# Optimization experiments

Measured on AMD Instinct MI355X. Metric: run time of the kernel, lower is better.

Reference implementation:

```python
import jax, jax.numpy as jnp
import numpy as np

N_NODES = 50000
N_EDGES = 800000
IN_FEATS, N_HIDDEN, N_CLASSES = 128, 128, 64
N_LAYERS = 3  # total GraphConv layers = N_LAYERS + 1


def setup_inputs() -> dict:
    key = jax.random.key(0)
    ks = jax.random.split(key, 16)
    features = jax.random.normal(ks[0], (N_NODES, IN_FEATS), dtype=jnp.float32)
    src = jax.random.randint(ks[1], (N_EDGES,), 0, N_NODES, dtype=jnp.int32)
    dst = jax.random.randint(ks[2], (N_EDGES,), 0, N_NODES, dtype=jnp.int32)
    def lin(k, fan_in, fan_out):
        s = 1.0 / np.sqrt(fan_in)
        return jax.random.uniform(k, (fan_in, fan_out), jnp.float32, -s, s)
    dims = [IN_FEATS] + [N_HIDDEN] * N_LAYERS + [N_CLASSES]
    inp = {"features": features, "src": src, "dst": dst}
    for i in range(len(dims) - 1):
        inp[f"W{i}"] = lin(ks[3 + i], dims[i], dims[i + 1])
        inp[f"b{i}"] = jnp.zeros((dims[i + 1],), jnp.float32)
    inp["Wp"] = lin(ks[10], N_CLASSES, 1)
    inp["bp"] = jnp.zeros((1,), jnp.float32)
    inp["Wv"] = lin(ks[11], N_CLASSES, 1)
    inp["bv"] = jnp.zeros((1,), jnp.float32)
    return inp


def _graph_conv(h, src, dst, norm_src, norm_dst, W, b, activate):
    # DGL GraphConv, norm='both': D_out^{-1/2} A D_in^{-1/2} X W + b
    h = h * norm_src  # [N, d]
    msg = h[src]      # [E, d] gather
    agg = jax.ops.segment_sum(msg, dst, num_segments=N_NODES)  # [N, d] scatter-add
    out = agg * norm_dst @ W + b
    return jax.nn.relu(out) if activate else out


def reference(features, src, dst, W0, b0, W1, b1, W2, b2, W3, b3, Wp, bp, Wv, bv):
    ones = jnp.ones((N_EDGES,), jnp.float32)
    out_deg = jax.ops.segment_sum(ones, src, num_segments=N_NODES)
    in_deg = jax.ops.segment_sum(ones, dst, num_segments=N_NODES)
    norm_src = jnp.clip(out_deg, 1.0) ** -0.5  # [N]
    norm_dst = jnp.clip(in_deg, 1.0) ** -0.5
    norm_src = norm_src[:, None]
    norm_dst = norm_dst[:, None]
    Ws = [W0, W1, W2, W3]
    bs = [b0, b1, b2, b3]
    h = features
    for i in range(4):
        h = _graph_conv(h, src, dst, norm_src, norm_dst, Ws[i], bs[i], activate=(i < 3))
    mN = jnp.sum(h, axis=0, keepdims=True)  # readout_nodes sum -> [1, n_classes]
    PI = h @ Wp + bp   # [N, 1]
    V = mN @ Wv + bv   # [1, 1]
    return (PI, V)
```

## Files before the change

### kernel.cpp

```cpp
#include <hip/hip_runtime.h>
#include <cstddef>

#define N_NODES 50000
#define N_EDGES 800000
#define NBUK    196
#define NBLK    256
#define EPB     3125
#define HEAD_BLOCKS 3136

typedef unsigned u32;
typedef unsigned short u16;
typedef __attribute__((ext_vector_type(8))) short bf16x8;
typedef __attribute__((ext_vector_type(4))) float f32x4;

__device__ __forceinline__ float bflo(u32 u) { return __uint_as_float(u << 16); }
__device__ __forceinline__ float bfhi(u32 u) { return __uint_as_float(u & 0xFFFF0000u); }
__device__ __forceinline__ u32 f2bf(float f) {
    u32 u = __float_as_uint(f);
    return (u + 0x7FFFu + ((u >> 16) & 1u)) >> 16;
}
__device__ __forceinline__ u32 packbf2(float a, float b) { return f2bf(a) | (f2bf(b) << 16); }

#define OFF_NS    0u
#define OFF_ND    200000u
#define OFF_RS    400000u
#define OFF_ES    600016u
#define OFF_CNTD  3800016u
#define OFF_CNTS  4000720u
#define OFF_TOTD  4201424u
#define OFF_TOTS  4202208u
#define OFF_BASED 4202992u
#define OFF_BASES 4203776u
#define OFF_VP    4204560u
#define OFF_DB    4217104u
#define OFF_SB    10617104u
#define OFF_T0    13817104u
#define OFF_T1    26617104u
#define OFF_TA    39417104u
#define OFF_TT    52217104u

__global__ __launch_bounds__(256)
void p1_kernel(const int* __restrict__ src, const int* __restrict__ dst,
               u32* __restrict__ cntD, u32* __restrict__ cntS) {
    __shared__ u32 dc[NBUK], sc[NBUK];
    int b = blockIdx.x, tid = threadIdx.x;
    if (tid < NBUK) { dc[tid] = 0; sc[tid] = 0; }
    __syncthreads();
    int lo = b * EPB, hi = lo + EPB;
    for (int e = lo + tid; e < hi; e += 256) {
        atomicAdd(&dc[dst[e] >> 8], 1u);
        atomicAdd(&sc[src[e] >> 8], 1u);
    }
    __syncthreads();
    if (tid < NBUK) {
        cntD[b * NBUK + tid] = dc[tid];
        cntS[b * NBUK + tid] = sc[tid];
    }
}

__global__ __launch_bounds__(256)
void p2a_kernel(u32* __restrict__ cntD, u32* __restrict__ cntS,
                u32* __restrict__ totD, u32* __restrict__ totS) {
    __shared__ u32 sc[256];
    int k = blockIdx.x, tid = threadIdx.x;
    u32 v = cntD[tid * NBUK + k];
    sc[tid] = v;
    __syncthreads();
    for (int o = 1; o < 256; o <<= 1) {
        u32 t = (tid >= o) ? sc[tid - o] : 0u;
        __syncthreads(); sc[tid] += t; __syncthreads();
    }
    cntD[tid * NBUK + k] = sc[tid] - v;
    if (tid == 255) totD[k] = sc[255];
    __syncthreads();
    v = cntS[tid * NBUK + k];
    sc[tid] = v;
    __syncthreads();
    for (int o = 1; o < 256; o <<= 1) {
        u32 t = (tid >= o) ? sc[tid - o] : 0u;
        __syncthreads(); sc[tid] += t; __syncthreads();
    }
    cntS[tid * NBUK + k] = sc[tid] - v;
    if (tid == 255) totS[k] = sc[255];
}

__global__ __launch_bounds__(256)
void p2b_kernel(const u32* __restrict__ totD, const u32* __restrict__ totS,
                u32* __restrict__ baseD, u32* __restrict__ baseS, u32* __restrict__ rs) {
    __shared__ u32 sc[256];
    int tid = threadIdx.x;
    u32 v = (tid < NBUK) ? totD[tid] : 0u;
    sc[tid] = v;
    __syncthreads();
    for (int o = 1; o < 256; o <<= 1) {
        u32 t = (tid >= o) ? sc[tid - o] : 0u;
        __syncthreads(); sc[tid] += t; __syncthreads();
    }
    if (tid < NBUK) baseD[tid] = sc[tid] - v;
    __syncthreads();
    v = (tid < NBUK) ? totS[tid] : 0u;
    sc[tid] = v;
    __syncthreads();
    for (int o = 1; o < 256; o <<= 1) {
        u32 t = (tid >= o) ? sc[tid - o] : 0u;
        __syncthreads(); sc[tid] += t; __syncthreads();
    }
    if (tid < NBUK) baseS[tid] = sc[tid] - v;
    if (tid == 0) rs[N_NODES] = N_EDGES;
}

__global__ __launch_bounds__(256)
void p3_kernel(const int* __restrict__ src, const int* __restrict__ dst,
               const u32* __restrict__ cntD, const u32* __restrict__ cntS,
               const u32* __restrict__ baseD, const u32* __restrict__ baseS,
               int2* __restrict__ db, int* __restrict__ sb) {
    __shared__ u32 od[NBUK], os[NBUK];
    int b = blockIdx.x, tid = threadIdx.x;
    if (tid < NBUK) {
        od[tid] = baseD[tid] + cntD[b * NBUK + tid];
        os[tid] = baseS[tid] + cntS[b * NBUK + tid];
    }
    __syncthreads();
    int lo = b * EPB, hi = lo + EPB;
    for (int e = lo + tid; e < hi; e += 256) {
        int s = src[e], d = dst[e];
        u32 p = atomicAdd(&od[d >> 8], 1u);
        db[p] = make_int2(s, d);
        u32 q = atomicAdd(&os[s >> 8], 1u);
        sb[q] = s;
    }
}

__global__ __launch_bounds__(256)
void p4d_kernel(const int2* __restrict__ db, const u32* __restrict__ totD,
                const u32* __restrict__ baseD, float* __restrict__ nd,
                u32* __restrict__ rs, int* __restrict__ es) {
    __shared__ u32 hist[256], sc[256], off[256];
    int k = blockIdx.x, tid = threadIdx.x;
    hist[tid] = 0;
    __syncthreads();
    u32 nEd = totD[k], base = baseD[k];
    for (u32 i = tid; i < nEd; i += 256)
        atomicAdd(&hist[db[base + i].y & 255], 1u);
    __syncthreads();
    u32 v = hist[tid];
    sc[tid] = v;
    __syncthreads();
    for (int o = 1; o < 256; o <<= 1) {
        u32 t = (tid >= o) ? sc[tid - o] : 0u;
        __syncthreads(); sc[tid] += t; __syncthreads();
    }
    u32 pf = sc[tid] - v;
    int node = k * 256 + tid;
    if (node < N_NODES) {
        rs[node] = base + pf;
        u32 c = v < 1u ? 1u : v;
        nd[node] = rsqrtf((float)c);
    }
    off[tid] = base + pf;
    __syncthreads();
    for (u32 i = tid; i < nEd; i += 256) {
        int2 p = db[base + i];
        u32 pos = atomicAdd(&off[p.y & 255], 1u);
        es[pos] = p.x;
    }
}

__global__ __launch_bounds__(256)
void p4sp_kernel(const int* __restrict__ sb, const u32* __restrict__ totS,
                 const u32* __restrict__ baseS, float* __restrict__ ns,
                 const float* __restrict__ feat, u16* __restrict__ hS) {
    __shared__ u32 hist[256];
    __shared__ float sns[256];
    int k = blockIdx.x, tid = threadIdx.x;
    hist[tid] = 0;
    __syncthreads();
    u32 n = totS[k], base = baseS[k];
    for (u32 i = tid; i < n; i += 256)
        atomicAdd(&hist[sb[base + i] & 255], 1u);
    __syncthreads();
    int node = k * 256 + tid;
    {
        u32 c = hist[tid]; if (c < 1u) c = 1u;
        float s = rsqrtf((float)c);
        sns[tid] = s;
        if (node < N_NODES) ns[node] = s;
    }
    __syncthreads();
    for (int i = tid; i < 256 * 32; i += 256) {
        int r = i >> 5, c4 = i & 31;
        int g = k * 256 + r;
        if (g >= N_NODES) break;
        float s = sns[r];
        float4 v = *(const float4*)&feat[(size_t)g * 128 + c4 * 4];
        uint2 o;
        o.x = packbf2(s * v.x, s * v.y);
        o.y = packbf2(s * v.z, s * v.w);
        *(uint2*)&hS[(size_t)g * 128 + c4 * 4] = o;
    }
}

__global__ __launch_bounds__(256)
void agg128_kernel(const u16* __restrict__ h, const u32* __restrict__ rs,
                   const int* __restrict__ es, u16* __restrict__ agg) {
    int node = blockIdx.x * 4 + (threadIdx.x >> 6);
    int lane = threadIdx.x & 63;
    int grp = lane >> 4;
    int q = lane & 15;
    const uint4* hp = (const uint4*)h;
    u32 s0 = rs[node], s1 = rs[node + 1];
    u32 deg = s1 - s0;
    u32 last = deg ? deg - 1u : 0u;
    float acc[8] = {0.f, 0.f, 0.f, 0.f, 0.f, 0.f, 0.f, 0.f};
    for (u32 b = 0; b < deg; b += 16) {
        u32 p0 = b + grp, p1 = b + 4 + grp, p2 = b + 8 + grp, p3 = b + 12 + grp;
        float m0 = p0 < deg ? 1.f : 0.f;  u32 x0 = p0 < deg ? p0 : last;
        float m1 = p1 < deg ? 1.f : 0.f;  u32 x1 = p1 < deg ? p1 : last;
        float m2 = p2 < deg ? 1.f : 0.f;  u32 x2 = p2 < deg ? p2 : last;
        float m3 = p3 < deg ? 1.f : 0.f;  u32 x3 = p3 < deg ? p3 : last;
        int e0 = es[s0 + x0], e1 = es[s0 + x1];
        int e2 = es[s0 + x2], e3 = es[s0 + x3];
        uint4 a = hp[(size_t)e0 * 16 + q];
        uint4 bb = hp[(size_t)e1 * 16 + q];
        uint4 c = hp[(size_t)e2 * 16 + q];
        uint4 d = hp[(size_t)e3 * 16 + q];
        acc[0] += m0 * bflo(a.x) + m1 * bflo(bb.x) + m2 * bflo(c.x) + m3 * bflo(d.x);
        acc[1] += m0 * bfhi(a.x) + m1 * bfhi(bb.x) + m2 * bfhi(c.x) + m3 * bfhi(d.x);
        acc[2] += m0 * bflo(a.y) + m1 * bflo(bb.y) + m2 * bflo(c.y) + m3 * bflo(d.y);
        acc[3] += m0 * bfhi(a.y) + m1 * bfhi(bb.y) + m2 * bfhi(c.y) + m3 * bfhi(d.y);
        acc[4] += m0 * bflo(a.z) + m1 * bflo(bb.z) + m2 * bflo(c.z) + m3 * bflo(d.z);
        acc[5] += m0 * bfhi(a.z) + m1 * bfhi(bb.z) + m2 * bfhi(c.z) + m3 * bfhi(d.z);
        acc[6] += m0 * bflo(a.w) + m1 * bflo(bb.w) + m2 * bflo(c.w) + m3 * bflo(d.w);
        acc[7] += m0 * bfhi(a.w) + m1 * bfhi(bb.w) + m2 * bfhi(c.w) + m3 * bfhi(d.w);
    }
    #pragma unroll
    for (int j = 0; j < 8; ++j) {
        acc[j] += __shfl_xor(acc[j], 16, 64);
        acc[j] += __shfl_xor(acc[j], 32, 64);
    }
    if (lane < 16) {
        uint4 pk;
        pk.x = packbf2(acc[0], acc[1]);
        pk.y = packbf2(acc[2], acc[3]);
        pk.z = packbf2(acc[4], acc[5]);
        pk.w = packbf2(acc[6], acc[7]);
        *(uint4*)&agg[(size_t)node * 128 + q * 8] = pk;
    }
}

template <int NCOL, int MODE>
__global__ __launch_bounds__(256)
void mfma_gemm_kernel(const u16* __restrict__ Ab, const float* __restrict__ W,
                      const float* __restrict__ bias, const float* __restrict__ ns,
                      const float* __restrict__ nd, u16* __restrict__ C) {
    constexpr int NT = NCOL / 16;
    constexpr int WROW = 136;
    constexpr int CROW = NCOL + 4;
    __shared__ u16 Wt[NCOL * WROW];
    __shared__ float Cl[4][16 * CROW];
    int tid = threadIdx.x;
    int w = tid >> 6, lane = tid & 63;
    int rowbase = blockIdx.x * 64 + w * 16;

    for (int i = tid; i < 64 * NCOL; i += 256) {
        int k2 = i / NCOL, c = i % NCOL;
        float w0 = W[(size_t)(2 * k2) * NCOL + c];
        float w1 = W[(size_t)(2 * k2 + 1) * NCOL + c];
        *(u32*)&Wt[c * WROW + 2 * k2] = packbf2(w0, w1);
    }
    __syncthreads();

    int m = lane & 15, kb = lane >> 4;
    int arow = rowbase + m;
    if (arow > N_NODES - 1) arow = N_NODES - 1;
    f32x4 acc[NT];
    #pragma unroll
    for (int nt = 0; nt < NT; ++nt) acc[nt] = (f32x4){0.f, 0.f, 0.f, 0.f};

    #pragma unroll
    for (int ks = 0; ks < 4; ++ks) {
        int k0 = ks * 32 + kb * 8;
        bf16x8 a = *(const bf16x8*)&Ab[(size_t)arow * 128 + k0];
        #pragma unroll
        for (int nt = 0; nt < NT; ++nt) {
            bf16x8 b = *(const bf16x8*)&Wt[(nt * 16 + m) * WROW + k0];
            acc[nt] = __builtin_amdgcn_mfma_f32_16x16x32_bf16(a, b, acc[nt], 0, 0, 0);
        }
    }

    #pragma unroll
    for (int nt = 0; nt < NT; ++nt)
        #pragma unroll
        for (int reg = 0; reg < 4; ++reg)
            Cl[w][(kb * 4 + reg) * CROW + nt * 16 + m] = acc[nt][reg];
    __syncthreads();

    constexpr int CQ = NCOL / 4;
    for (int i = lane; i < 16 * CQ; i += 64) {
        int r = i / CQ, c4 = (i % CQ) * 4;
        int row = rowbase + r;
        if (row < N_NODES) {
            float4 o = *(float4*)&Cl[w][r * CROW + c4];
            if (MODE == 0) {
                float sd = nd[row], ss = ns[row];
                o.x = ss * fmaxf(sd * o.x + bias[c4 + 0], 0.f);
                o.y = ss * fmaxf(sd * o.y + bias[c4 + 1], 0.f);
                o.z = ss * fmaxf(sd * o.z + bias[c4 + 2], 0.f);
                o.w = ss * fmaxf(sd * o.w + bias[c4 + 3], 0.f);
            }
            uint2 pk = {packbf2(o.x, o.y), packbf2(o.z, o.w)};
            *(uint2*)&C[(size_t)row * NCOL + c4] = pk;
        }
    }
}

__global__ __launch_bounds__(256)
void l3head_kernel(const u16* __restrict__ t, const u32* __restrict__ rs,
                   const int* __restrict__ es, const float* __restrict__ nd,
                   const float* __restrict__ b3, const float* __restrict__ Wp,
                   const float* __restrict__ Wv, const float* __restrict__ bp,
                   float* __restrict__ out, float* __restrict__ vpart) {
    __shared__ float sv;
    if (threadIdx.x == 0) sv = 0.f;
    __syncthreads();
    int lane = threadIdx.x & 63;
    int wvid = threadIdx.x >> 6;
    int oct = lane >> 3;
    int q = lane & 7;
    const uint4* hp = (const uint4*)t;
    float4 b3a = ((const float4*)b3)[q * 2];
    float4 b3b = ((const float4*)b3)[q * 2 + 1];
    float4 wpa = ((const float4*)Wp)[q * 2];
    float4 wpb = ((const float4*)Wp)[q * 2 + 1];
    float4 wva = ((const float4*)Wv)[q * 2];
    float4 wvb = ((const float4*)Wv)[q * 2 + 1];
    float bpv = bp[0];
    float vacc = 0.f;
    for (int n = blockIdx.x * 4 + wvid; n < N_NODES; n += HEAD_BLOCKS * 4) {
        u32 s0 = rs[n], s1 = rs[n + 1];
        u32 deg = s1 - s0;
        u32 last = deg ? deg - 1u : 0u;
        float acc[8] = {0.f, 0.f, 0.f, 0.f, 0.f, 0.f, 0.f, 0.f};
        for (u32 b = 0; b < deg; b += 32) {
            u32 p0 = b + oct, p1 = b + 8 + oct, p2 = b + 16 + oct, p3 = b + 24 + oct;
            float m0 = p0 < deg ? 1.f : 0.f;  u32 x0 = p0 < deg ? p0 : last;
            float m1 = p1 < deg ? 1.f : 0.f;  u32 x1 = p1 < deg ? p1 : last;
            float m2 = p2 < deg ? 1.f : 0.f;  u32 x2 = p2 < deg ? p2 : last;
            float m3 = p3 < deg ? 1.f : 0.f;  u32 x3 = p3 < deg ? p3 : last;
            int e0 = es[s0 + x0], e1 = es[s0 + x1];
            int e2 = es[s0 + x2], e3 = es[s0 + x3];
            uint4 a = hp[(size_t)e0 * 8 + q];
            uint4 bb = hp[(size_t)e1 * 8 + q];
            uint4 c = hp[(size_t)e2 * 8 + q];
            uint4 d = hp[(size_t)e3 * 8 + q];
            acc[0] += m0 * bflo(a.x) + m1 * bflo(bb.x) + m2 * bflo(c.x) + m3 * bflo(d.x);
            acc[1] += m0 * bfhi(a.x) + m1 * bfhi(bb.x) + m2 * bfhi(c.x) + m3 * bfhi(d.x);
            acc[2] += m0 * bflo(a.y) + m1 * bflo(bb.y) + m2 * bflo(c.y) + m3 * bflo(d.y);
            acc[3] += m0 * bfhi(a.y) + m1 * bfhi(bb.y) + m2 * bfhi(c.y) + m3 * bfhi(d.y);
            acc[4] += m0 * bflo(a.z) + m1 * bflo(bb.z) + m2 * bflo(c.z) + m3 * bflo(d.z);
            acc[5] += m0 * bfhi(a.z) + m1 * bfhi(bb.z) + m2 * bfhi(c.z) + m3 * bfhi(d.z);
            acc[6] += m0 * bflo(a.w) + m1 * bflo(bb.w) + m2 * bflo(c.w) + m3 * bflo(d.w);
            acc[7] += m0 * bfhi(a.w) + m1 * bfhi(bb.w) + m2 * bfhi(c.w) + m3 * bfhi(d.w);
        }
        #pragma unroll
        for (int j = 0; j < 8; ++j) {
            acc[j] += __shfl_xor(acc[j], 8, 64);
            acc[j] += __shfl_xor(acc[j], 16, 64);
            acc[j] += __shfl_xor(acc[j], 32, 64);
        }
        float ndv = nd[n];
        float h0 = ndv * acc[0] + b3a.x, h1 = ndv * acc[1] + b3a.y;
        float h2 = ndv * acc[2] + b3a.z, h3 = ndv * acc[3] + b3a.w;
        float h4 = ndv * acc[4] + b3b.x, h5 = ndv * acc[5] + b3b.y;
        float h6 = ndv * acc[6] + b3b.z, h7 = ndv * acc[7] + b3b.w;
        float p  = h0 * wpa.x + h1 * wpa.y + h2 * wpa.z + h3 * wpa.w
                 + h4 * wpb.x + h5 * wpb.y + h6 * wpb.z + h7 * wpb.w;
        float vv = h0 * wva.x + h1 * wva.y + h2 * wva.z + h3 * wva.w
                 + h4 * wvb.x + h5 * wvb.y + h6 * wvb.z + h7 * wvb.w;
        p  += __shfl_xor(p, 1, 64);  p  += __shfl_xor(p, 2, 64);  p  += __shfl_xor(p, 4, 64);
        vv += __shfl_xor(vv, 1, 64); vv += __shfl_xor(vv, 2, 64); vv += __shfl_xor(vv, 4, 64);
        if (lane == 0) { out[n] = p + bpv; vacc += vv; }
    }
    if (lane == 0) atomicAdd(&sv, vacc);
    __syncthreads();
    if (threadIdx.x == 0) vpart[blockIdx.x] = sv;
}

__global__ __launch_bounds__(256)
void vred_kernel(const float* __restrict__ vpart, const float* __restrict__ bv,
                 float* __restrict__ out) {
    float v = 0.f;
    for (int i = threadIdx.x; i < HEAD_BLOCKS; i += 256) v += vpart[i];
    #pragma unroll
    for (int off = 32; off; off >>= 1) v += __shfl_down(v, off, 64);
    __shared__ float s[4];
    if ((threadIdx.x & 63) == 0) s[threadIdx.x >> 6] = v;
    __syncthreads();
    if (threadIdx.x == 0) out[N_NODES] = s[0] + s[1] + s[2] + s[3] + bv[0];
}

extern "C" void kernel_launch(void* const* d_in, const int* in_sizes, int n_in,
                              void* d_out, int out_size, void* d_ws, size_t ws_size,
                              hipStream_t stream) {
    const float* feat = (const float*)d_in[0];
    const int*   src  = (const int*)d_in[1];
    const int*   dst  = (const int*)d_in[2];
    const float* W0 = (const float*)d_in[3];  const float* b0 = (const float*)d_in[4];
    const float* W1 = (const float*)d_in[5];  const float* b1 = (const float*)d_in[6];
    const float* W2 = (const float*)d_in[7];  const float* b2 = (const float*)d_in[8];
    const float* W3 = (const float*)d_in[9];  const float* b3 = (const float*)d_in[10];
    const float* Wp = (const float*)d_in[11]; const float* bp = (const float*)d_in[12];
    const float* Wv = (const float*)d_in[13]; const float* bv = (const float*)d_in[14];
    float* out = (float*)d_out;
    char*  wsb = (char*)d_ws;

    float* ns    = (float*)(wsb + OFF_NS);
    float* nd    = (float*)(wsb + OFF_ND);
    u32*   rs    = (u32*)(wsb + OFF_RS);
    int*   es    = (int*)(wsb + OFF_ES);
    u32*   cntD  = (u32*)(wsb + OFF_CNTD);
    u32*   cntS  = (u32*)(wsb + OFF_CNTS);
    u32*   totD  = (u32*)(wsb + OFF_TOTD);
    u32*   totS  = (u32*)(wsb + OFF_TOTS);
    u32*   baseD = (u32*)(wsb + OFF_BASED);
    u32*   baseS = (u32*)(wsb + OFF_BASES);
    float* vpart = (float*)(wsb + OFF_VP);
    int2*  db    = (int2*)(wsb + OFF_DB);
    int*   sb    = (int*)(wsb + OFF_SB);
    u16*   T0    = (u16*)(wsb + OFF_T0);
    u16*   T1    = (u16*)(wsb + OFF_T1);
    u16*   TA    = (u16*)(wsb + OFF_TA);
    u16*   Tt    = (u16*)(wsb + OFF_TT);

    p1_kernel<<<NBLK, 256, 0, stream>>>(src, dst, cntD, cntS);
    p2a_kernel<<<NBUK, 256, 0, stream>>>(cntD, cntS, totD, totS);
    p2b_kernel<<<1, 256, 0, stream>>>(totD, totS, baseD, baseS, rs);
    p3_kernel<<<NBLK, 256, 0, stream>>>(src, dst, cntD, cntS, baseD, baseS, db, sb);
    p4d_kernel<<<NBUK, 256, 0, stream>>>(db, totD, baseD, nd, rs, es);
    p4sp_kernel<<<NBUK, 256, 0, stream>>>(sb, totS, baseS, ns, feat, T0);

    agg128_kernel<<<12500, 256, 0, stream>>>(T0, rs, es, TA);
    mfma_gemm_kernel<128, 0><<<782, 256, 0, stream>>>(TA, W0, b0, ns, nd, T1);
    agg128_kernel<<<12500, 256, 0, stream>>>(T1, rs, es, TA);
    mfma_gemm_kernel<128, 0><<<782, 256, 0, stream>>>(TA, W1, b1, ns, nd, T0);
    agg128_kernel<<<12500, 256, 0, stream>>>(T0, rs, es, TA);
    mfma_gemm_kernel<128, 0><<<782, 256, 0, stream>>>(TA, W2, b2, ns, nd, T1);
    mfma_gemm_kernel<64, 1><<<782, 256, 0, stream>>>(T1, W3, b3, ns, nd, Tt);
    l3head_kernel<<<HEAD_BLOCKS, 256, 0, stream>>>(Tt, rs, es, nd, b3, Wp, Wv, bp, out, vpart);
    vred_kernel<<<1, 256, 0, stream>>>(vpart, bv, out);
}
```

Before: 350.6 us.

## Compress edge index buffers to narrow types and drop masked aggregation tails

Source indices in the CSR edge list are now stored as u16, since node ids fit in 16 bits. The bucketing intermediates are packed too: src<<8 | dst-low-byte goes into one u32, and the src bucket array holds only a u8 low byte. This cuts the bytes written and read by the preprocessing passes and by every aggregation's index loads. The aggregation and head kernels replace the masked, clamped loop with a full-chunk loop plus an 8- or 4-wide loop and a predicated remainder, removing the per-edge multiply-by-mask work. The u16 encoding relies on N_NODES staying below 65536.

```diff
diff --git a/kernel.cpp b/kernel.cpp
--- a/kernel.cpp
+++ b/kernel.cpp
@@ -10,6 +10,7 @@
 
 typedef unsigned u32;
 typedef unsigned short u16;
+typedef unsigned char u8;
 typedef __attribute__((ext_vector_type(8))) short bf16x8;
 typedef __attribute__((ext_vector_type(4))) float f32x4;
 
@@ -25,19 +26,19 @@
 #define OFF_ND    200000u
 #define OFF_RS    400000u
 #define OFF_ES    600016u
-#define OFF_CNTD  3800016u
-#define OFF_CNTS  4000720u
-#define OFF_TOTD  4201424u
-#define OFF_TOTS  4202208u
-#define OFF_BASED 4202992u
-#define OFF_BASES 4203776u
-#define OFF_VP    4204560u
-#define OFF_DB    4217104u
-#define OFF_SB    10617104u
-#define OFF_T0    13817104u
-#define OFF_T1    26617104u
-#define OFF_TA    39417104u
-#define OFF_TT    52217104u
+#define OFF_CNTD  2200016u
+#define OFF_CNTS  2400720u
+#define OFF_TOTD  2601424u
+#define OFF_TOTS  2602208u
+#define OFF_BASED 2602992u
+#define OFF_BASES 2603776u
+#define OFF_VP    2604560u
+#define OFF_DB    2617104u
+#define OFF_SB    5817104u
+#define OFF_T0    6617104u
+#define OFF_T1    19417104u
+#define OFF_TA    32217104u
+#define OFF_TT    45017104u
 
 __global__ __launch_bounds__(256)
 void p1_kernel(const int* __restrict__ src, const int* __restrict__ dst,
@@ -113,7 +114,7 @@
 void p3_kernel(const int* __restrict__ src, const int* __restrict__ dst,
                const u32* __restrict__ cntD, const u32* __restrict__ cntS,
                const u32* __restrict__ baseD, const u32* __restrict__ baseS,
-               int2* __restrict__ db, int* __restrict__ sb) {
+               u32* __restrict__ db, u8* __restrict__ sb) {
     __shared__ u32 od[NBUK], os[NBUK];
     int b = blockIdx.x, tid = threadIdx.x;
     if (tid < NBUK) {
@@ -125,23 +126,23 @@
     for (int e = lo + tid; e < hi; e += 256) {
         int s = src[e], d = dst[e];
         u32 p = atomicAdd(&od[d >> 8], 1u);
-        db[p] = make_int2(s, d);
+        db[p] = ((u32)s << 8) | (u32)(d & 255);
         u32 q = atomicAdd(&os[s >> 8], 1u);
-        sb[q] = s;
-    }
-}
-
-__global__ __launch_bounds__(256)
-void p4d_kernel(const int2* __restrict__ db, const u32* __restrict__ totD,
+        sb[q] = (u8)(s & 255);
+    }
+}
+
+__global__ __launch_bounds__(256)
+void p4d_kernel(const u32* __restrict__ db, const u32* __restrict__ totD,
                 const u32* __restrict__ baseD, float* __restrict__ nd,
-                u32* __restrict__ rs, int* __restrict__ es) {
+                u32* __restrict__ rs, u16* __restrict__ es) {
     __shared__ u32 hist[256], sc[256], off[256];
     int k = blockIdx.x, tid = threadIdx.x;
     hist[tid] = 0;
     __syncthreads();
     u32 nEd = totD[k], base = baseD[k];
     for (u32 i = tid; i < nEd; i += 256)
-        atomicAdd(&hist[db[base + i].y & 255], 1u);
+        atomicAdd(&hist[db[base + i] & 255u], 1u);
     __syncthreads();
     u32 v = hist[tid];
     sc[tid] = v;
@@ -160,14 +161,14 @@
     off[tid] = base + pf;
     __syncthreads();
     for (u32 i = tid; i < nEd; i += 256) {
-        int2 p = db[base + i];
-        u32 pos = atomicAdd(&off[p.y & 255], 1u);
-        es[pos] = p.x;
-    }
-}
-
-__global__ __launch_bounds__(256)
-void p4sp_kernel(const int* __restrict__ sb, const u32* __restrict__ totS,
+        u32 p = db[base + i];
+        u32 pos = atomicAdd(&off[p & 255u], 1u);
+        es[pos] = (u16)(p >> 8);
+    }
+}
+
+__global__ __launch_bounds__(256)
+void p4sp_kernel(const u8* __restrict__ sb, const u32* __restrict__ totS,
                  const u32* __restrict__ baseS, float* __restrict__ ns,
                  const float* __restrict__ feat, u16* __restrict__ hS) {
     __shared__ u32 hist[256];
@@ -177,7 +178,7 @@
     __syncthreads();
     u32 n = totS[k], base = baseS[k];
     for (u32 i = tid; i < n; i += 256)
-        atomicAdd(&hist[sb[base + i] & 255], 1u);
+        atomicAdd(&hist[sb[base + i]], 1u);
     __syncthreads();
     int node = k * 256 + tid;
     {
@@ -202,36 +203,45 @@
 
 __global__ __launch_bounds__(256)
 void agg128_kernel(const u16* __restrict__ h, const u32* __restrict__ rs,
-                   const int* __restrict__ es, u16* __restrict__ agg) {
+                   const u16* __restrict__ es, u16* __restrict__ agg) {
     int node = blockIdx.x * 4 + (threadIdx.x >> 6);
     int lane = threadIdx.x & 63;
-    int grp = lane >> 4;
+    int quarter = lane >> 4;
     int q = lane & 15;
     const uint4* hp = (const uint4*)h;
     u32 s0 = rs[node], s1 = rs[node + 1];
-    u32 deg = s1 - s0;
-    u32 last = deg ? deg - 1u : 0u;
     float acc[8] = {0.f, 0.f, 0.f, 0.f, 0.f, 0.f, 0.f, 0.f};
-    for (u32 b = 0; b < deg; b += 16) {
-        u32 p0 = b + grp, p1 = b + 4 + grp, p2 = b + 8 + grp, p3 = b + 12 + grp;
-        float m0 = p0 < deg ? 1.f : 0.f;  u32 x0 = p0 < deg ? p0 : last;
-        float m1 = p1 < deg ? 1.f : 0.f;  u32 x1 = p1 < deg ? p1 : last;
-        float m2 = p2 < deg ? 1.f : 0.f;  u32 x2 = p2 < deg ? p2 : last;
-        float m3 = p3 < deg ? 1.f : 0.f;  u32 x3 = p3 < deg ? p3 : last;
-        int e0 = es[s0 + x0], e1 = es[s0 + x1];
-        int e2 = es[s0 + x2], e3 = es[s0 + x3];
+    u32 i = s0;
+    for (; i + 16 <= s1; i += 16) {
+        int e0 = es[i + quarter],     e1 = es[i + 4 + quarter];
+        int e2 = es[i + 8 + quarter], e3 = es[i + 12 + quarter];
         uint4 a = hp[(size_t)e0 * 16 + q];
-        uint4 bb = hp[(size_t)e1 * 16 + q];
+        uint4 b = hp[(size_t)e1 * 16 + q];
         uint4 c = hp[(size_t)e2 * 16 + q];
         uint4 d = hp[(size_t)e3 * 16 + q];
-        acc[0] += m0 * bflo(a.x) + m1 * bflo(bb.x) + m2 * bflo(c.x) + m3 * bflo(d.x);
-        acc[1] += m0 * bfhi(a.x) + m1 * bfhi(bb.x) + m2 * bfhi(c.x) + m3 * bfhi(d.x);
-        acc[2] += m0 * bflo(a.y) + m1 * bflo(bb.y) + m2 * bflo(c.y) + m3 * bflo(d.y);
-        acc[3] += m0 * bfhi(a.y) + m1 * bfhi(bb.y) + m2 * bfhi(c.y) + m3 * bfhi(d.y);
-        acc[4] += m0 * bflo(a.z) + m1 * bflo(bb.z) + m2 * bflo(c.z) + m3 * bflo(d.z);
-        acc[5] += m0 * bfhi(a.z) + m1 * bfhi(bb.z) + m2 * bfhi(c.z) + m3 * bfhi(d.z);
-        acc[6] += m0 * bflo(a.w) + m1 * bflo(bb.w) + m2 * bflo(c.w) + m3 * bflo(d.w);
-        acc[7] += m0 * bfhi(a.w) + m1 * bfhi(bb.w) + m2 * bfhi(c.w) + m3 * bfhi(d.w);
+        acc[0] += (bflo(a.x) + bflo(b.x)) + (bflo(c.x) + bflo(d.x));
+        acc[1] += (bfhi(a.x) + bfhi(b.x)) + (bfhi(c.x) + bfhi(d.x));
+        acc[2] += (bflo(a.y) + bflo(b.y)) + (bflo(c.y) + bflo(d.y));
+        acc[3] += (bfhi(a.y) + bfhi(b.y)) + (bfhi(c.y) + bfhi(d.y));
+        acc[4] += (bflo(a.z) + bflo(b.z)) + (bflo(c.z) + bflo(d.z));
+        acc[5] += (bfhi(a.z) + bfhi(b.z)) + (bfhi(c.z) + bfhi(d.z));
+        acc[6] += (bflo(a.w) + bflo(b.w)) + (bflo(c.w) + bflo(d.w));
+        acc[7] += (bfhi(a.w) + bfhi(b.w)) + (bfhi(c.w) + bfhi(d.w));
+    }
+    for (; i + 4 <= s1; i += 4) {
+        uint4 a = hp[(size_t)es[i + quarter] * 16 + q];
+        acc[0] += bflo(a.x); acc[1] += bfhi(a.x);
+        acc[2] += bflo(a.y); acc[3] += bfhi(a.y);
+        acc[4] += bflo(a.z); acc[5] += bfhi(a.z);
+        acc[6] += bflo(a.w); acc[7] += bfhi(a.w);
+    }
+    u32 rem = s1 - i;
+    if ((u32)quarter < rem) {
+        uint4 a = hp[(size_t)es[i + quarter] * 16 + q];
+        acc[0] += bflo(a.x); acc[1] += bfhi(a.x);
+        acc[2] += bflo(a.y); acc[3] += bfhi(a.y);
+        acc[4] += bflo(a.z); acc[5] += bfhi(a.z);
+        acc[6] += bflo(a.w); acc[7] += bfhi(a.w);
     }
     #pragma unroll
     for (int j = 0; j < 8; ++j) {
@@ -316,7 +326,7 @@
 
 __global__ __launch_bounds__(256)
 void l3head_kernel(const u16* __restrict__ t, const u32* __restrict__ rs,
-                   const int* __restrict__ es, const float* __restrict__ nd,
+                   const u16* __restrict__ es, const float* __restrict__ nd,
                    const float* __restrict__ b3, const float* __restrict__ Wp,
                    const float* __restrict__ Wv, const float* __restrict__ bp,
                    float* __restrict__ out, float* __restrict__ vpart) {
@@ -338,29 +348,38 @@
     float vacc = 0.f;
     for (int n = blockIdx.x * 4 + wvid; n < N_NODES; n += HEAD_BLOCKS * 4) {
         u32 s0 = rs[n], s1 = rs[n + 1];
-        u32 deg = s1 - s0;
-        u32 last = deg ? deg - 1u : 0u;
         float acc[8] = {0.f, 0.f, 0.f, 0.f, 0.f, 0.f, 0.f, 0.f};
-        for (u32 b = 0; b < deg; b += 32) {
-            u32 p0 = b + oct, p1 = b + 8 + oct, p2 = b + 16 + oct, p3 = b + 24 + oct;
-            float m0 = p0 < deg ? 1.f : 0.f;  u32 x0 = p0 < deg ? p0 : last;
-            float m1 = p1 < deg ? 1.f : 0.f;  u32 x1 = p1 < deg ? p1 : last;
-            float m2 = p2 < deg ? 1.f : 0.f;  u32 x2 = p2 < deg ? p2 : last;
-            float m3 = p3 < deg ? 1.f : 0.f;  u32 x3 = p3 < deg ? p3 : last;
-            int e0 = es[s0 + x0], e1 = es[s0 + x1];
-            int e2 = es[s0 + x2], e3 = es[s0 + x3];
+        u32 i = s0;
+        for (; i + 32 <= s1; i += 32) {
+            int e0 = es[i + oct],      e1 = es[i + 8 + oct];
+            int e2 = es[i + 16 + oct], e3 = es[i + 24 + oct];
             uint4 a = hp[(size_t)e0 * 8 + q];
             uint4 bb = hp[(size_t)e1 * 8 + q];
             uint4 c = hp[(size_t)e2 * 8 + q];
             uint4 d = hp[(size_t)e3 * 8 + q];
-            acc[0] += m0 * bflo(a.x) + m1 * bflo(bb.x) + m2 * bflo(c.x) + m3 * bflo(d.x);
-            acc[1] += m0 * bfhi(a.x) + m1 * bfhi(bb.x) + m2 * bfhi(c.x) + m3 * bfhi(d.x);
-            acc[2] += m0 * bflo(a.y) + m1 * bflo(bb.y) + m2 * bflo(c.y) + m3 * bflo(d.y);
-            acc[3] += m0 * bfhi(a.y) + m1 * bfhi(bb.y) + m2 * bfhi(c.y) + m3 * bfhi(d.y);
-            acc[4] += m0 * bflo(a.z) + m1 * bflo(bb.z) + m2 * bflo(c.z) + m3 * bflo(d.z);
-            acc[5] += m0 * bfhi(a.z) + m1 * bfhi(bb.z) + m2 * bfhi(c.z) + m3 * bfhi(d.z);
-            acc[6] += m0 * bflo(a.w) + m1 * bflo(bb.w) + m2 * bflo(c.w) + m3 * bflo(d.w);
-            acc[7] += m0 * bfhi(a.w) + m1 * bfhi(bb.w) + m2 * bfhi(c.w) + m3 * bfhi(d.w);
+            acc[0] += (bflo(a.x) + bflo(bb.x)) + (bflo(c.x) + bflo(d.x));
+            acc[1] += (bfhi(a.x) + bfhi(bb.x)) + (bfhi(c.x) + bfhi(d.x));
+            acc[2] += (bflo(a.y) + bflo(bb.y)) + (bflo(c.y) + bflo(d.y));
+            acc[3] += (bfhi(a.y) + bfhi(bb.y)) + (bfhi(c.y) + bfhi(d.y));
+            acc[4] += (bflo(a.z) + bflo(bb.z)) + (bflo(c.z) + bflo(d.z));
+            acc[5] += (bfhi(a.z) + bfhi(bb.z)) + (bfhi(c.z) + bfhi(d.z));
+            acc[6] += (bflo(a.w) + bflo(bb.w)) + (bflo(c.w) + bflo(d.w));
+            acc[7] += (bfhi(a.w) + bfhi(bb.w)) + (bfhi(c.w) + bfhi(d.w));
+        }
+        for (; i + 8 <= s1; i += 8) {
+            uint4 a = hp[(size_t)es[i + oct] * 8 + q];
+            acc[0] += bflo(a.x); acc[1] += bfhi(a.x);
+            acc[2] += bflo(a.y); acc[3] += bfhi(a.y);
+            acc[4] += bflo(a.z); acc[5] += bfhi(a.z);
+            acc[6] += bflo(a.w); acc[7] += bfhi(a.w);
+        }
+        u32 rem = s1 - i;
+        if ((u32)oct < rem) {
+            uint4 a = hp[(size_t)es[i + oct] * 8 + q];
+            acc[0] += bflo(a.x); acc[1] += bfhi(a.x);
+            acc[2] += bflo(a.y); acc[3] += bfhi(a.y);
+            acc[4] += bflo(a.z); acc[5] += bfhi(a.z);
+            acc[6] += bflo(a.w); acc[7] += bfhi(a.w);
         }
         #pragma unroll
         for (int j = 0; j < 8; ++j) {
@@ -417,7 +436,7 @@
     float* ns    = (float*)(wsb + OFF_NS);
     float* nd    = (float*)(wsb + OFF_ND);
     u32*   rs    = (u32*)(wsb + OFF_RS);
-    int*   es    = (int*)(wsb + OFF_ES);
+    u16*   es    = (u16*)(wsb + OFF_ES);
     u32*   cntD  = (u32*)(wsb + OFF_CNTD);
     u32*   cntS  = (u32*)(wsb + OFF_CNTS);
     u32*   totD  = (u32*)(wsb + OFF_TOTD);
@@ -425,8 +444,8 @@
     u32*   baseD = (u32*)(wsb + OFF_BASED);
     u32*   baseS = (u32*)(wsb + OFF_BASES);
     float* vpart = (float*)(wsb + OFF_VP);
-    int2*  db    = (int2*)(wsb + OFF_DB);
-    int*   sb    = (int*)(wsb + OFF_SB);
+    u32*   db    = (u32*)(wsb + OFF_DB);
+    u8*    sb    = (u8*)(wsb + OFF_SB);
     u16*   T0    = (u16*)(wsb + OFF_T0);
     u16*   T1    = (u16*)(wsb + OFF_T1);
     u16*   TA    = (u16*)(wsb + OFF_TA);
```

Result: no change. 355.1 us (+1.3%).
